# Optimization experiments

Hardware: AMD Instinct MI355X
Metric: run time of the kernel (lower is better)

## Reference

```python
import jax, jax.numpy as jnp
import numpy as np

NUM_CLASSES = 96
T = 27          # max label slots per sample (hardcoded `range(1, 27)` in source)
NEG = -1e9      # finite stand-in for -inf masking (sim values are in [-1, 1])


def setup_inputs() -> dict:
    key = jax.random.key(0)
    k1, k2, k3 = jax.random.split(key, 3)
    B, D = 256, 1024
    input_f = jax.random.normal(k1, (B, T, D), dtype=jnp.float32)
    # labels in [1, 95]; zero is the end-of-word terminator
    tgt = jax.random.randint(k2, (B, T), 1, NUM_CLASSES, dtype=jnp.int32)
    lens = jax.random.randint(k3, (B,), 5, T, dtype=jnp.int32)  # first zero at position lens >= 1
    tgt = jnp.where(jnp.arange(T)[None, :] >= lens[:, None], 0, tgt)
    return {"input_f": input_f, "target": tgt}


def reference(input_f, target):
    B, Tt, D = input_f.shape
    # first zero position in target[:, 1:] gives the ragged prefix length per sample
    fz = jnp.argmax(target[:, 1:] == 0, axis=1) + 1            # [B], in [1, T-1]
    valid = jnp.arange(Tt)[None, :] < fz[:, None]              # [B, T] prefix mask (t=0 always valid)
    m = valid.reshape(-1)                                      # [B*T]

    # L2-normalize all rows (padded rows are masked out of the loss below)
    f = input_f.reshape(-1, D)
    f = f / jnp.clip(jnp.linalg.norm(f, axis=1, keepdims=True), 1e-12)
    sim = f @ f.T                                              # [N, N], N = B*T

    lab = target.reshape(-1)
    same = lab[:, None] == lab[None, :]                        # label_encode @ label_encode.T == 1
    pair_valid = m[:, None] & m[None, :]

    eye = jnp.eye(m.shape[0], dtype=bool)
    # multi-positive cross entropy (QDTrack-style):
    # loss_i = log(1 + sum_{pos p, neg n} exp(sim_in - sim_ip))
    #        = softplus(logsumexp_n(sim_in) + logsumexp_p(-sim_ip))
    pos_mask = (pair_valid & same) | (~m[:, None] & eye)       # give invalid rows a dummy entry
    neg_mask = (pair_valid & ~same) | (~m[:, None] & eye)
    lse_pos = jax.nn.logsumexp(jnp.where(pos_mask, -sim, NEG), axis=1)
    lse_neg = jax.nn.logsumexp(jnp.where(neg_mask, sim, NEG), axis=1)
    row_loss = jax.nn.softplus(lse_pos + lse_neg)

    n_valid = jnp.sum(m.astype(sim.dtype))
    return jnp.sum(jnp.where(m, row_loss, 0.0)) / n_valid
```

## Files before the change

### kernel.cpp

```cpp
#include <hip/hip_runtime.h>
#include <hip/hip_bf16.h>
#include <stdint.h>

#define BATCH 256
#define TSLOT 27
#define NTOT  (BATCH * TSLOT)
#define DIM   1024
#define BM    128
#define NTILES 54
#define NTRI  (NTILES * (NTILES + 1) / 2)
#define KST   16

typedef __attribute__((ext_vector_type(4))) float f32x4;
typedef __attribute__((ext_vector_type(2))) long l64x2;

__global__ __launch_bounds__(256) void prepscan_kernel(const int* __restrict__ tgt,
                                                       int* __restrict__ offs,
                                                       int* __restrict__ meta,
                                                       int* __restrict__ clab,
                                                       float* __restrict__ accum,
                                                       int* __restrict__ counter) {
    int b = threadIdx.x;
    const int* t = tgt + b * TSLOT;
    int fz = 1;
    for (int i = 1; i < TSLOT; ++i) {
        if (t[i] == 0) { fz = i; break; }
    }
    __shared__ int sh[256];
    sh[b] = fz;
    __syncthreads();
    for (int d = 1; d < 256; d <<= 1) {
        int v = (b >= d) ? sh[b - d] : 0;
        __syncthreads();
        sh[b] += v;
        __syncthreads();
    }
    offs[b] = sh[b] - fz;
    if (b < 2) accum[b] = 0.0f;
    if (b == 2) *counter = 0;
    __syncthreads();
    int nv = sh[255];
    int npad = ((nv + 127) / 128) * 128;
    if (b == 255) {
        offs[256] = nv;
        meta[0] = nv;
        meta[1] = npad;
    }
    if (b < npad - nv) clab[nv + b] = -1;
}

__global__ __launch_bounds__(256) void norm_c_kernel(const float* __restrict__ in,
                                                     const int* __restrict__ tgt,
                                                     const int* __restrict__ offs,
                                                     unsigned char* __restrict__ cfb,
                                                     int* __restrict__ clab) {
    const int wv   = blockIdx.x * 4 + (threadIdx.x >> 6);
    const int lane = threadIdx.x & 63;
    const int b = wv / TSLOT, t = wv - b * TSLOT;
    const int o0 = offs[b], o1 = offs[b + 1];
    if (t >= o1 - o0) return;
    const int dest = o0 + t;
    const float* src = in + (size_t)wv * DIM + lane * 16;
    float4 v0 = *(const float4*)(src);
    float4 v1 = *(const float4*)(src + 4);
    float4 v2 = *(const float4*)(src + 8);
    float4 v3 = *(const float4*)(src + 12);
    float ss = v0.x*v0.x + v0.y*v0.y + v0.z*v0.z + v0.w*v0.w
             + v1.x*v1.x + v1.y*v1.y + v1.z*v1.z + v1.w*v1.w
             + v2.x*v2.x + v2.y*v2.y + v2.z*v2.z + v2.w*v2.w
             + v3.x*v3.x + v3.y*v3.y + v3.z*v3.z + v3.w*v3.w;
    #pragma unroll
    for (int off = 1; off < 64; off <<= 1) ss += __shfl_xor(ss, off);
    const float sc = 1.0f / fmaxf(sqrtf(ss), 1e-12f);
    float f[16] = {v0.x,v0.y,v0.z,v0.w, v1.x,v1.y,v1.z,v1.w,
                   v2.x,v2.y,v2.z,v2.w, v3.x,v3.y,v3.z,v3.w};
    uint4 o;
    unsigned int* ow = (unsigned int*)&o;
    #pragma unroll
    for (int q = 0; q < 4; ++q) {
        unsigned int u = 0;
        u = __builtin_amdgcn_cvt_pk_fp8_f32(f[q*4+0] * sc, f[q*4+1] * sc, u, 0);
        u = __builtin_amdgcn_cvt_pk_fp8_f32(f[q*4+2] * sc, f[q*4+3] * sc, u, 1);
        ow[q] = u;
    }
    *(uint4*)(cfb + (size_t)dest * DIM + lane * 16) = o;
    if (lane == 0) clab[dest] = tgt[wv];
}

__global__ __launch_bounds__(512) void gemm_kernel(const unsigned char* __restrict__ fb,
                                                   const int* __restrict__ clab,
                                                   const int* __restrict__ meta,
                                                   float* __restrict__ Ppos,
                                                   float* __restrict__ Pneg) {
    __shared__ __align__(16) char lds[49152];

    int t = blockIdx.x;
    int bi = 0;
    while (t >= NTILES - bi) { t -= NTILES - bi; ++bi; }
    const int bj = bi + t;
    const int npad = meta[1];
    const int col0 = bj * BM;
    if (col0 >= npad) return;
    const int row0 = bi * BM;
    const bool diag = (bi == bj);

    const int tid  = threadIdx.x;
    const int lane = tid & 63;
    const int w    = tid >> 6;
    const int wm   = w & 1;
    const int wn   = w >> 1;

    f32x4 acc[4][2] = {};
    const char* fbyte = (const char*)fb;

    auto stage = [&](int s) {
        char* buf = lds + (s % 3) * 16384;
        const int k0b = s * 64;
        const int c = w * 64 + lane;
        const int r = c >> 2, ks = c & 3;
        const int srcoff = ((ks ^ ((r >> 1) & 3)) << 4);
        const char* ga = fbyte + (size_t)(row0 + r) * DIM + k0b + srcoff;
        __builtin_amdgcn_global_load_lds(
            (const __attribute__((address_space(1))) void*)ga,
            (__attribute__((address_space(3))) void*)(buf + c * 16),
            16, 0, 0);
        const char* gb = fbyte + (size_t)(col0 + r) * DIM + k0b + srcoff;
        __builtin_amdgcn_global_load_lds(
            (const __attribute__((address_space(1))) void*)gb,
            (__attribute__((address_space(3))) void*)(buf + 8192 + c * 16),
            16, 0, 0);
    };

    const int rsel = lane & 15, tsl = lane >> 4;
    auto compute = [&](int s) {
        const char* bA = lds + (s % 3) * 16384;
        const char* bB = bA + 8192;
        l64x2 av[4], bv[2];
        #pragma unroll
        for (int m = 0; m < 4; ++m) {
            const int r = wm * 64 + m * 16 + rsel;
            av[m] = *(const l64x2*)(bA + r * 64 + ((tsl ^ ((r >> 1) & 3)) << 4));
        }
        #pragma unroll
        for (int n = 0; n < 2; ++n) {
            const int r = wn * 32 + n * 16 + rsel;
            bv[n] = *(const l64x2*)(bB + r * 64 + ((tsl ^ ((r >> 1) & 3)) << 4));
        }
        #pragma unroll
        for (int kk = 0; kk < 2; ++kk)
            #pragma unroll
            for (int m = 0; m < 4; ++m)
                #pragma unroll
                for (int n = 0; n < 2; ++n)
                    acc[m][n] = __builtin_amdgcn_mfma_f32_16x16x32_fp8_fp8(
                        av[m][kk], bv[n][kk], acc[m][n], 0, 0, 0);
    };

    stage(0); stage(1);
    #pragma unroll 1
    for (int s = 0; s < KST - 2; ++s) {
        asm volatile("s_waitcnt vmcnt(2)" ::: "memory");
        __builtin_amdgcn_s_barrier();
        asm volatile("" ::: "memory");
        stage(s + 2);
        compute(s);
    }
    asm volatile("s_waitcnt vmcnt(2)" ::: "memory");
    __builtin_amdgcn_s_barrier();
    asm volatile("" ::: "memory");
    compute(KST - 2);
    asm volatile("s_waitcnt vmcnt(0)" ::: "memory");
    __builtin_amdgcn_s_barrier();
    asm volatile("" ::: "memory");
    compute(KST - 1);

    const int c = rsel, g = tsl;
    float cpos[2] = {0, 0}, cneg[2] = {0, 0};
    float* fl = (float*)(lds + 16384);

    #pragma unroll
    for (int m = 0; m < 4; ++m) {
        #pragma unroll
        for (int rg = 0; rg < 4; ++rg) {
            const int gi = row0 + wm * 64 + m * 16 + g * 4 + rg;
            const int li = clab[gi];
            float rp = 0.0f, rn = 0.0f;
            #pragma unroll
            for (int n = 0; n < 2; ++n) {
                const int gj = col0 + wn * 32 + n * 16 + c;
                const int lj = clab[gj];
                const float s = acc[m][n][rg];
                if (li >= 0 && lj >= 0) {
                    if (li == lj) { float e = __expf(-s); rp += e; cpos[n] += e; }
                    else          { float e = __expf(s);  rn += e; cneg[n] += e; }
                }
            }
            #pragma unroll
            for (int off = 1; off <= 8; off <<= 1) {
                rp += __shfl_xor(rp, off);
                rn += __shfl_xor(rn, off);
            }
            if (c == 0) {
                int lr = m * 16 + g * 4 + rg;
                fl[w * 64 + lr]        = rp;
                fl[512 + w * 64 + lr]  = rn;
            }
        }
    }
    #pragma unroll
    for (int n = 0; n < 2; ++n) {
        float p = cpos[n], q = cneg[n];
        p += __shfl_xor(p, 16); p += __shfl_xor(p, 32);
        q += __shfl_xor(q, 16); q += __shfl_xor(q, 32);
        if (g == 0) {
            int lc = n * 16 + c;
            fl[1024 + w * 32 + lc] = p;
            fl[1280 + w * 32 + lc] = q;
        }
    }
    __syncthreads();
    if (tid < 128) {
        int sm = tid >> 6, lr = tid & 63;
        float rp = 0.0f, rn = 0.0f;
        #pragma unroll
        for (int k = 0; k < 4; ++k) {
            rp += fl[(sm + 2 * k) * 64 + lr];
            rn += fl[512 + (sm + 2 * k) * 64 + lr];
        }
        int gi = row0 + tid;
        Ppos[(size_t)bj * NTOT + gi] = rp;
        Pneg[(size_t)bj * NTOT + gi] = rn;
    } else if (tid < 256 && !diag) {
        int j = tid - 128, cn = j >> 5, lc = j & 31;
        float p = fl[1024 + (cn * 2) * 32 + lc] + fl[1024 + (cn * 2 + 1) * 32 + lc];
        float q = fl[1280 + (cn * 2) * 32 + lc] + fl[1280 + (cn * 2 + 1) * 32 + lc];
        int gj = col0 + j;
        Ppos[(size_t)bi * NTOT + gj] = p;
        Pneg[(size_t)bi * NTOT + gj] = q;
    }
}

__global__ __launch_bounds__(256) void finalize_kernel(const int* __restrict__ clab,
                                                       const int* __restrict__ meta,
                                                       const float* __restrict__ Ppos,
                                                       const float* __restrict__ Pneg,
                                                       float* __restrict__ accum,
                                                       int* __restrict__ counter,
                                                       float* __restrict__ out) {
    int i = blockIdx.x * blockDim.x + threadIdx.x;
    const int npad = meta[1];
    const int nta = npad >> 7;
    float s = 0.0f, cnt = 0.0f;
    if (i < npad && clab[i] >= 0) {
        float sp = 0.0f, sn = 0.0f;
        for (int t = 0; t < nta; ++t) {
            sp += Ppos[(size_t)t * NTOT + i];
            sn += Pneg[(size_t)t * NTOT + i];
        }
        s = log1pf(sp * sn);
        cnt = 1.0f;
    }
    #pragma unroll
    for (int off = 1; off < 64; off <<= 1) {
        s   += __shfl_xor(s, off);
        cnt += __shfl_xor(cnt, off);
    }
    __shared__ float sh[8];
    int lane = threadIdx.x & 63, w = threadIdx.x >> 6;
    if (lane == 0) { sh[w] = s; sh[4 + w] = cnt; }
    __syncthreads();
    if (threadIdx.x == 0) {
        atomicAdd(&accum[0], sh[0] + sh[1] + sh[2] + sh[3]);
        atomicAdd(&accum[1], sh[4] + sh[5] + sh[6] + sh[7]);
        __threadfence();
        int done = atomicAdd(counter, 1);
        if (done == (int)gridDim.x - 1) {
            __threadfence();
            out[0] = accum[0] / accum[1];
        }
    }
}

extern "C" void kernel_launch(void* const* d_in, const int* in_sizes, int n_in,
                              void* d_out, int out_size, void* d_ws, size_t ws_size,
                              hipStream_t stream) {
    (void)in_sizes; (void)n_in; (void)out_size; (void)ws_size;
    const float* input_f = (const float*)d_in[0];
    const int*   target  = (const int*)d_in[1];
    float* out = (float*)d_out;

    char* ws = (char*)d_ws;
    const size_t FB_BYTES = (size_t)NTOT * DIM;
    unsigned char* cfb = (unsigned char*)ws;
    char* p = ws + FB_BYTES;
    int*   clab  = (int*)p;            p += NTOT * 4;
    int*   offs  = (int*)p;            p += 4096;
    int*   meta  = (int*)p;            p += 256;
    float* accum = (float*)p;          p += 128;
    int*   counter = (int*)p;          p += 128;
    float* Ppos  = (float*)p;          p += (size_t)NTILES * NTOT * 4;
    float* Pneg  = (float*)p;

    prepscan_kernel<<<dim3(1), dim3(256), 0, stream>>>(target, offs, meta, clab, accum, counter);
    norm_c_kernel<<<dim3(NTOT / 4), dim3(256), 0, stream>>>(input_f, target, offs, cfb, clab);
    gemm_kernel<<<dim3(NTRI), dim3(512), 0, stream>>>(cfb, clab, meta, Ppos, Pneg);
    finalize_kernel<<<dim3((NTOT + 255) / 256), dim3(256), 0, stream>>>(clab, meta, Ppos, Pneg, accum, counter, out);
}
```

Baseline: 56.39 us.

## Enlarge GEMM tiles to 192, deepen LDS pipeline, remap blocks across XCDs

Output tiles grow from 128x128 to 192x192, with each wave holding a 6x3 block of MFMA accumulators. The LDS ring goes from three to four stages, so each loop step waits with vmcnt(6) instead of vmcnt(2). Blocks are assigned by an XCD-strided index over only the active triangle tiles, computed from the runtime npad, and npad is now padded to 192. The aim is more operand reuse per LDS byte and less global traffic, at the cost of fewer, heavier blocks, higher register and LDS use (96KB per block), and more padded rows.

```diff
diff --git a/kernel.cpp b/kernel.cpp
--- a/kernel.cpp
+++ b/kernel.cpp
@@ -6,10 +6,11 @@
 #define TSLOT 27
 #define NTOT  (BATCH * TSLOT)
 #define DIM   1024
-#define BM    128
-#define NTILES 54
-#define NTRI  (NTILES * (NTILES + 1) / 2)
+#define TS    192
+#define NSMAX 36
+#define NTRIMAX (NSMAX * (NSMAX + 1) / 2)
 #define KST   16
+#define BUFSZ 24576
 
 typedef __attribute__((ext_vector_type(4))) float f32x4;
 typedef __attribute__((ext_vector_type(2))) long l64x2;
@@ -40,7 +41,7 @@
     if (b == 2) *counter = 0;
     __syncthreads();
     int nv = sh[255];
-    int npad = ((nv + 127) / 128) * 128;
+    int npad = ((nv + TS - 1) / TS) * TS;
     if (b == 255) {
         offs[256] = nv;
         meta[0] = nv;
@@ -92,80 +93,89 @@
                                                    const int* __restrict__ meta,
                                                    float* __restrict__ Ppos,
                                                    float* __restrict__ Pneg) {
-    __shared__ __align__(16) char lds[49152];
-
-    int t = blockIdx.x;
+    __shared__ __align__(16) char lds[4 * BUFSZ];
+
+    const int npad = meta[1];
+    const int nstrips = npad / TS;
+    const int nact = nstrips * (nstrips + 1) / 2;
+    const int k = blockIdx.x >> 3, x = blockIdx.x & 7;
+    const int q8 = nact >> 3, r8 = nact & 7;
+    const int cnt = q8 + (x < r8 ? 1 : 0);
+    if (k >= cnt) return;
+    int t = x * q8 + (x < r8 ? x : r8) + k;
     int bi = 0;
-    while (t >= NTILES - bi) { t -= NTILES - bi; ++bi; }
+    while (t >= nstrips - bi) { t -= nstrips - bi; ++bi; }
     const int bj = bi + t;
-    const int npad = meta[1];
-    const int col0 = bj * BM;
-    if (col0 >= npad) return;
-    const int row0 = bi * BM;
+    const int row0 = bi * TS;
+    const int col0 = bj * TS;
     const bool diag = (bi == bj);
 
     const int tid  = threadIdx.x;
     const int lane = tid & 63;
     const int w    = tid >> 6;
-    const int wm   = w & 1;
-    const int wn   = w >> 1;
-
-    f32x4 acc[4][2] = {};
+    const int wm   = w >> 2;
+    const int wn   = w & 3;
+
+    f32x4 acc[6][3] = {};
     const char* fbyte = (const char*)fb;
 
     auto stage = [&](int s) {
-        char* buf = lds + (s % 3) * 16384;
+        char* buf = lds + (s & 3) * BUFSZ;
         const int k0b = s * 64;
-        const int c = w * 64 + lane;
-        const int r = c >> 2, ks = c & 3;
-        const int srcoff = ((ks ^ ((r >> 1) & 3)) << 4);
-        const char* ga = fbyte + (size_t)(row0 + r) * DIM + k0b + srcoff;
-        __builtin_amdgcn_global_load_lds(
-            (const __attribute__((address_space(1))) void*)ga,
-            (__attribute__((address_space(3))) void*)(buf + c * 16),
-            16, 0, 0);
-        const char* gb = fbyte + (size_t)(col0 + r) * DIM + k0b + srcoff;
-        __builtin_amdgcn_global_load_lds(
-            (const __attribute__((address_space(1))) void*)gb,
-            (__attribute__((address_space(3))) void*)(buf + 8192 + c * 16),
-            16, 0, 0);
+        #pragma unroll
+        for (int j = 0; j < 3; ++j) {
+            const int c = w * 192 + j * 64 + lane;
+            const int cc = (c >= 768) ? c - 768 : c;
+            const int base = (c >= 768) ? col0 : row0;
+            const int r = cc >> 2, ks = cc & 3;
+            const int srcoff = ((ks ^ ((r >> 1) & 3)) << 4);
+            const char* g = fbyte + (size_t)(base + r) * DIM + k0b + srcoff;
+            __builtin_amdgcn_global_load_lds(
+                (const __attribute__((address_space(1))) void*)g,
+                (__attribute__((address_space(3))) void*)(buf + c * 16),
+                16, 0, 0);
+        }
     };
 
     const int rsel = lane & 15, tsl = lane >> 4;
     auto compute = [&](int s) {
-        const char* bA = lds + (s % 3) * 16384;
-        const char* bB = bA + 8192;
-        l64x2 av[4], bv[2];
-        #pragma unroll
-        for (int m = 0; m < 4; ++m) {
-            const int r = wm * 64 + m * 16 + rsel;
+        const char* bA = lds + (s & 3) * BUFSZ;
+        const char* bB = bA + 12288;
+        l64x2 av[6], bv[3];
+        #pragma unroll
+        for (int m = 0; m < 6; ++m) {
+            const int r = wm * 96 + m * 16 + rsel;
             av[m] = *(const l64x2*)(bA + r * 64 + ((tsl ^ ((r >> 1) & 3)) << 4));
         }
         #pragma unroll
-        for (int n = 0; n < 2; ++n) {
-            const int r = wn * 32 + n * 16 + rsel;
+        for (int n = 0; n < 3; ++n) {
+            const int r = wn * 48 + n * 16 + rsel;
             bv[n] = *(const l64x2*)(bB + r * 64 + ((tsl ^ ((r >> 1) & 3)) << 4));
         }
         #pragma unroll
         for (int kk = 0; kk < 2; ++kk)
             #pragma unroll
-            for (int m = 0; m < 4; ++m)
+            for (int m = 0; m < 6; ++m)
                 #pragma unroll
-                for (int n = 0; n < 2; ++n)
+                for (int n = 0; n < 3; ++n)
                     acc[m][n] = __builtin_amdgcn_mfma_f32_16x16x32_fp8_fp8(
                         av[m][kk], bv[n][kk], acc[m][n], 0, 0, 0);
     };
 
-    stage(0); stage(1);
+    stage(0); stage(1); stage(2);
     #pragma unroll 1
-    for (int s = 0; s < KST - 2; ++s) {
-        asm volatile("s_waitcnt vmcnt(2)" ::: "memory");
+    for (int s = 0; s < KST - 3; ++s) {
+        asm volatile("s_waitcnt vmcnt(6)" ::: "memory");
         __builtin_amdgcn_s_barrier();
         asm volatile("" ::: "memory");
-        stage(s + 2);
+        stage(s + 3);
         compute(s);
     }
-    asm volatile("s_waitcnt vmcnt(2)" ::: "memory");
+    asm volatile("s_waitcnt vmcnt(6)" ::: "memory");
+    __builtin_amdgcn_s_barrier();
+    asm volatile("" ::: "memory");
+    compute(KST - 3);
+    asm volatile("s_waitcnt vmcnt(3)" ::: "memory");
     __builtin_amdgcn_s_barrier();
     asm volatile("" ::: "memory");
     compute(KST - 2);
@@ -175,19 +185,19 @@
     compute(KST - 1);
 
     const int c = rsel, g = tsl;
-    float cpos[2] = {0, 0}, cneg[2] = {0, 0};
-    float* fl = (float*)(lds + 16384);
-
-    #pragma unroll
-    for (int m = 0; m < 4; ++m) {
+    float cpos[3] = {0, 0, 0}, cneg[3] = {0, 0, 0};
+    float* fl = (float*)lds;
+
+    #pragma unroll
+    for (int m = 0; m < 6; ++m) {
         #pragma unroll
         for (int rg = 0; rg < 4; ++rg) {
-            const int gi = row0 + wm * 64 + m * 16 + g * 4 + rg;
+            const int gi = row0 + wm * 96 + m * 16 + g * 4 + rg;
             const int li = clab[gi];
             float rp = 0.0f, rn = 0.0f;
             #pragma unroll
-            for (int n = 0; n < 2; ++n) {
-                const int gj = col0 + wn * 32 + n * 16 + c;
+            for (int n = 0; n < 3; ++n) {
+                const int gj = col0 + wn * 48 + n * 16 + c;
                 const int lj = clab[gj];
                 const float s = acc[m][n][rg];
                 if (li >= 0 && lj >= 0) {
@@ -202,38 +212,38 @@
             }
             if (c == 0) {
                 int lr = m * 16 + g * 4 + rg;
-                fl[w * 64 + lr]        = rp;
-                fl[512 + w * 64 + lr]  = rn;
+                fl[w * 96 + lr]        = rp;
+                fl[768 + w * 96 + lr]  = rn;
             }
         }
     }
     #pragma unroll
-    for (int n = 0; n < 2; ++n) {
+    for (int n = 0; n < 3; ++n) {
         float p = cpos[n], q = cneg[n];
         p += __shfl_xor(p, 16); p += __shfl_xor(p, 32);
         q += __shfl_xor(q, 16); q += __shfl_xor(q, 32);
         if (g == 0) {
             int lc = n * 16 + c;
-            fl[1024 + w * 32 + lc] = p;
-            fl[1280 + w * 32 + lc] = q;
+            fl[1536 + w * 48 + lc] = p;
+            fl[1920 + w * 48 + lc] = q;
         }
     }
     __syncthreads();
-    if (tid < 128) {
-        int sm = tid >> 6, lr = tid & 63;
+    if (tid < 192) {
+        int sm = tid / 96, lr = tid % 96;
         float rp = 0.0f, rn = 0.0f;
         #pragma unroll
-        for (int k = 0; k < 4; ++k) {
-            rp += fl[(sm + 2 * k) * 64 + lr];
-            rn += fl[512 + (sm + 2 * k) * 64 + lr];
+        for (int kk = 0; kk < 4; ++kk) {
+            rp += fl[(sm * 4 + kk) * 96 + lr];
+            rn += fl[768 + (sm * 4 + kk) * 96 + lr];
         }
         int gi = row0 + tid;
         Ppos[(size_t)bj * NTOT + gi] = rp;
         Pneg[(size_t)bj * NTOT + gi] = rn;
-    } else if (tid < 256 && !diag) {
-        int j = tid - 128, cn = j >> 5, lc = j & 31;
-        float p = fl[1024 + (cn * 2) * 32 + lc] + fl[1024 + (cn * 2 + 1) * 32 + lc];
-        float q = fl[1280 + (cn * 2) * 32 + lc] + fl[1280 + (cn * 2 + 1) * 32 + lc];
+    } else if (tid < 384 && !diag) {
+        int j = tid - 192, cn = j / 48, lc = j % 48;
+        float p = fl[1536 + cn * 48 + lc] + fl[1536 + (4 + cn) * 48 + lc];
+        float q = fl[1920 + cn * 48 + lc] + fl[1920 + (4 + cn) * 48 + lc];
         int gj = col0 + j;
         Ppos[(size_t)bi * NTOT + gj] = p;
         Pneg[(size_t)bi * NTOT + gj] = q;
@@ -249,7 +259,7 @@
                                                        float* __restrict__ out) {
     int i = blockIdx.x * blockDim.x + threadIdx.x;
     const int npad = meta[1];
-    const int nta = npad >> 7;
+    const int nta = npad / TS;
     float s = 0.0f, cnt = 0.0f;
     if (i < npad && clab[i] >= 0) {
         float sp = 0.0f, sn = 0.0f;
@@ -298,11 +308,11 @@
     int*   meta  = (int*)p;            p += 256;
     float* accum = (float*)p;          p += 128;
     int*   counter = (int*)p;          p += 128;
-    float* Ppos  = (float*)p;          p += (size_t)NTILES * NTOT * 4;
+    float* Ppos  = (float*)p;          p += (size_t)NSMAX * NTOT * 4;
     float* Pneg  = (float*)p;
 
     prepscan_kernel<<<dim3(1), dim3(256), 0, stream>>>(target, offs, meta, clab, accum, counter);
     norm_c_kernel<<<dim3(NTOT / 4), dim3(256), 0, stream>>>(input_f, target, offs, cfb, clab);
-    gemm_kernel<<<dim3(NTRI), dim3(512), 0, stream>>>(cfb, clab, meta, Ppos, Pneg);
+    gemm_kernel<<<dim3(NTRIMAX), dim3(512), 0, stream>>>(cfb, clab, meta, Ppos, Pneg);
     finalize_kernel<<<dim3((NTOT + 255) / 256), dim3(256), 0, stream>>>(clab, meta, Ppos, Pneg, accum, counter, out);
 }
```

After: 51.02 us. 9.5% less time.
